# Kernel tuning notes

Hardware: AMD Instinct MI355X
Metric: run time of the kernel (lower is better)

Reference implementation:

```python
import jax, jax.numpy as jnp
import numpy as np

NC = 80            # num_classes
REG_MAX = 16
STRIDES = (8, 16, 32)
IMG = 640.0
TOPK = 10
TAL_ALPHA = 0.5
TAL_BETA = 6.0
L_BOX, L_CLS, L_DFL = 7.5, 0.5, 1.5
EPS = 1e-9
NEG = -1e8


def bbox_iou(b1, b2, ciou=False, eps=1e-7):
    # b1, b2: (..., 4) xyxy, broadcastable
    inter_wh = jnp.clip(jnp.minimum(b1[..., 2:], b2[..., 2:]) - jnp.maximum(b1[..., :2], b2[..., :2]), 0.0)
    inter = inter_wh[..., 0] * inter_wh[..., 1]
    w1 = jnp.clip(b1[..., 2] - b1[..., 0], 0.0); h1 = jnp.clip(b1[..., 3] - b1[..., 1], 0.0)
    w2 = jnp.clip(b2[..., 2] - b2[..., 0], 0.0); h2 = jnp.clip(b2[..., 3] - b2[..., 1], 0.0)
    union = w1 * h1 + w2 * h2 - inter + eps
    iou = inter / union
    if not ciou:
        return iou
    cx1 = (b1[..., 0] + b1[..., 2]) * 0.5; cy1 = (b1[..., 1] + b1[..., 3]) * 0.5
    cx2 = (b2[..., 0] + b2[..., 2]) * 0.5; cy2 = (b2[..., 1] + b2[..., 3]) * 0.5
    rho2 = (cx2 - cx1) ** 2 + (cy2 - cy1) ** 2
    cw = jnp.maximum(b1[..., 2], b2[..., 2]) - jnp.minimum(b1[..., 0], b2[..., 0])
    ch = jnp.maximum(b1[..., 3], b2[..., 3]) - jnp.minimum(b1[..., 1], b2[..., 1])
    c2 = cw ** 2 + ch ** 2 + eps
    v = (4.0 / np.pi ** 2) * (jnp.arctan(w2 / (h2 + eps)) - jnp.arctan(w1 / (h1 + eps))) ** 2
    alpha = jax.lax.stop_gradient(v / (1.0 - iou + v + eps))  # torch computes alpha under no_grad
    return iou - (rho2 / c2 + alpha * v)


def _assign_one(pred_scores, pred_bboxes, anchor_points, gt_labels, gt_bboxes):
    """TaskAlignedAssigner for one image.
    pred_scores (N,nc), pred_bboxes (N,4), anchor_points (N,2), gt_labels (M,), gt_bboxes (M,4).
    Returns target_bboxes (N,4), target_scores (N,nc), fg_mask (N,)."""
    N = pred_bboxes.shape[0]; M = gt_bboxes.shape[0]
    gl = jnp.clip(gt_labels.astype(jnp.int32), 0, NC - 1)
    x = anchor_points[:, 0]; y = anchor_points[:, 1]
    l = x[:, None] - gt_bboxes[None, :, 0]
    t = y[:, None] - gt_bboxes[None, :, 1]
    r = gt_bboxes[None, :, 2] - x[:, None]
    b = gt_bboxes[None, :, 3] - y[:, None]
    in_gts = (l > 0) & (t > 0) & (r > 0) & (b > 0)                     # (N,M)
    ious = bbox_iou(pred_bboxes[:, None, :], gt_bboxes[None, :, :])    # (N,M)
    cls_score = pred_scores[:, gl]                                     # (N,M)
    align = jnp.clip(cls_score, 0.0) ** TAL_ALPHA * jnp.clip(ious, 0.0) ** TAL_BETA
    align = jnp.where(in_gts, align, NEG)
    k = min(TOPK, N)
    _, topk_idx = jax.lax.top_k(align.T, k)                            # (M,k) indices into N
    mask_topk = jnp.zeros((M, N), dtype=bool).at[jnp.arange(M)[:, None], topk_idx].set(True).T
    mask_pos = mask_topk & in_gts                                      # (N,M)
    ious_pos = jnp.where(mask_pos, ious, -1.0)
    max_iou = ious_pos.max(axis=1)
    gt_idx = ious_pos.argmax(axis=1)                                   # (N,)
    fg_mask = max_iou > -0.5
    metric_pos = jnp.where(mask_pos, align, NEG)
    metric_max = jnp.clip(metric_pos.max(axis=0), EPS)                 # (M,)
    rows = jnp.arange(N)
    score = align[rows, gt_idx] / metric_max[gt_idx] * ious[rows, gt_idx]
    score = jnp.clip(score, 0.0, 1.0) * fg_mask.astype(pred_scores.dtype)
    tcls = gl[gt_idx]
    target_scores = jnp.zeros((N, NC), dtype=pred_scores.dtype).at[rows, tcls].set(score)
    target_bboxes = jnp.where(fg_mask[:, None], gt_bboxes[gt_idx], 0.0)
    return target_bboxes, target_scores, fg_mask


def _df_loss(reg_logits, target):
    # reg_logits (B,N,4,R) logits, target (B,N,4) float in [0,R-1] -> (B,N)
    t = jnp.clip(target, 0.0, float(REG_MAX - 1))
    left = jnp.floor(t).astype(jnp.int32)
    right = jnp.minimum(left + 1, REG_MAX - 1)
    wl = right.astype(t.dtype) - t
    wr = t - left.astype(t.dtype)
    same = right == left
    wl = jnp.where(same, 1.0, wl)
    wr = jnp.where(same, 0.0, wr)
    logp = jax.nn.log_softmax(reg_logits, axis=-1)
    ll = -jnp.take_along_axis(logp, left[..., None], axis=-1)[..., 0]
    lr = -jnp.take_along_axis(logp, right[..., None], axis=-1)[..., 0]
    return (ll * wl + lr * wr).sum(axis=-1)


def _forward(p0, p1, p2, gt_bboxes, gt_labels):
    preds = [p0, p1, p2]
    B = p0.shape[0]
    reg_ch = 4 * REG_MAX
    cls_list, reg_list, ap_list, st_list = [], [], [], []
    for p, s in zip(preds, STRIDES):
        _, _, h, w = p.shape
        reg = p[:, :reg_ch]
        cls = p[:, reg_ch:]
        cls_list.append(cls.transpose(0, 2, 3, 1).reshape(B, -1, NC))
        reg_list.append(reg.transpose(0, 2, 3, 1).reshape(B, -1, 4, REG_MAX))
        gy, gx = jnp.meshgrid(jnp.arange(h), jnp.arange(w), indexing='ij')
        pts = jnp.stack([(gx + 0.5) * s, (gy + 0.5) * s], axis=-1).reshape(-1, 2).astype(p.dtype)
        ap_list.append(pts)
        st_list.append(jnp.full((h * w,), float(s), dtype=p.dtype))
    cls_logits = jnp.concatenate(cls_list, axis=1)      # (B,N,nc)
    reg_logits = jnp.concatenate(reg_list, axis=1)      # (B,N,4,R)
    anchor_points = jnp.concatenate(ap_list, axis=0)    # (N,2)
    stride_t = jnp.concatenate(st_list, axis=0)         # (N,)
    pred_scores = jax.nn.sigmoid(cls_logits)
    proj = jnp.arange(REG_MAX, dtype=cls_logits.dtype)
    dist = (jax.nn.softmax(reg_logits, axis=-1) * proj).sum(-1) * stride_t[None, :, None]  # (B,N,4)
    ax = anchor_points[:, 0]; ay = anchor_points[:, 1]
    pred_bboxes = jnp.stack([ax - dist[..., 0], ay - dist[..., 1], ax + dist[..., 2], ay + dist[..., 3]], axis=-1)
    # --- TAL assignment (runs under no_grad in torch) ---
    tb, ts, fg = jax.vmap(lambda ps, pb, gl, gb: _assign_one(ps, pb, anchor_points, gl, gb))(
        jax.lax.stop_gradient(pred_scores), jax.lax.stop_gradient(pred_bboxes), gt_labels, gt_bboxes)
    tb = jax.lax.stop_gradient(tb)
    ts = jax.lax.stop_gradient(ts)
    ts_sum = jnp.maximum(ts.sum(), 1.0)
    # --- cls: BCE with logits over all anchors/classes ---
    z = cls_logits
    bce = jnp.clip(z, 0.0) - z * ts + jnp.log1p(jnp.exp(-jnp.abs(z)))
    loss_cls = bce.sum() / ts_sum
    # --- box: CIoU weighted by target score, fg only ---
    weight = ts.sum(-1) * fg.astype(ts.dtype)           # (B,N)
    ciou = bbox_iou(pred_bboxes, tb, ciou=True)         # (B,N)
    loss_box = ((1.0 - ciou) * weight).sum() / ts_sum
    # --- dfl ---
    inv_s = 1.0 / stride_t
    tl = (ax - tb[..., 0]) * inv_s
    tt = (ay - tb[..., 1]) * inv_s
    tr = (tb[..., 2] - ax) * inv_s
    tbm = (tb[..., 3] - ay) * inv_s
    target_ltrb = jnp.clip(jnp.stack([tl, tt, tr, tbm], axis=-1), 0.0, float(REG_MAX - 1))
    dfl = _df_loss(reg_logits, target_ltrb)             # (B,N)
    loss_dfl = (dfl * weight).sum() / ts_sum
    return L_BOX * loss_box + L_CLS * loss_cls + L_DFL * loss_dfl


def setup_inputs() -> dict:
    key = jax.random.key(0)
    k0, k1, k2, kc, kw, kl = jax.random.split(key, 6)
    B, C = 16, 4 * REG_MAX + NC
    p0 = jax.random.normal(k0, (B, C, 80, 80), dtype=jnp.float32)
    p1 = jax.random.normal(k1, (B, C, 40, 40), dtype=jnp.float32)
    p2 = jax.random.normal(k2, (B, C, 20, 20), dtype=jnp.float32)
    M = 32
    cxy = jax.random.uniform(kc, (B, M, 2), minval=64.0, maxval=IMG - 64.0)
    wh = jax.random.uniform(kw, (B, M, 2), minval=16.0, maxval=128.0)
    gt_bboxes = jnp.concatenate([cxy - wh * 0.5, cxy + wh * 0.5], axis=-1).astype(jnp.float32)
    gt_labels = jax.random.randint(kl, (B, M), 0, NC, dtype=jnp.int32).astype(jnp.int64)
    return {"p0": p0, "p1": p1, "p2": p2, "gt_bboxes": gt_bboxes, "gt_labels": gt_labels}


def reference(p0, p1, p2, gt_bboxes, gt_labels):
    return _forward(p0, p1, p2, gt_bboxes, gt_labels)
```

## Files before the change

### kernel.cpp

```cpp
#include <hip/hip_runtime.h>

#define BATCH 16
#define NANCH 8400
#define MGT 32
#define NCLS 80
#define RCH 64
#define NCH 144
#define TOPKK 10
#define MAXC 576
#define PBLK 2100
#define BCEB 2625
#define TOTB (PBLK + BCEB)

struct AInfo { int lvl, pos, W, HW; float s, ax, ay; };

__device__ __forceinline__ AInfo anchor_of(int n) {
  AInfo a;
  if (n < 6400)      { a.lvl = 0; a.pos = n;        a.W = 80; a.HW = 6400; a.s = 8.f;  }
  else if (n < 8000) { a.lvl = 1; a.pos = n - 6400; a.W = 40; a.HW = 1600; a.s = 16.f; }
  else               { a.lvl = 2; a.pos = n - 8000; a.W = 20; a.HW = 400;  a.s = 32.f; }
  int px = a.pos % a.W, py = a.pos / a.W;
  a.ax = (px + 0.5f) * a.s;
  a.ay = (py + 0.5f) * a.s;
  return a;
}

__device__ __forceinline__ const float* lvl_ptr(const float* p0, const float* p1,
                                                const float* p2, int lvl) {
  return lvl == 0 ? p0 : (lvl == 1 ? p1 : p2);
}

__device__ __forceinline__ float iou_xyxy(float4 a, float4 b) {
  float ix = fmaxf(fminf(a.z, b.z) - fmaxf(a.x, b.x), 0.f);
  float iy = fmaxf(fminf(a.w, b.w) - fmaxf(a.y, b.y), 0.f);
  float inter = ix * iy;
  float w1 = fmaxf(a.z - a.x, 0.f), h1 = fmaxf(a.w - a.y, 0.f);
  float w2 = fmaxf(b.z - b.x, 0.f), h2 = fmaxf(b.w - b.y, 0.f);
  float uni = w1 * h1 + w2 * h2 - inter + 1e-7f;
  return inter / uni;
}

__device__ __forceinline__ float ciou_xyxy(float4 a, float4 b) {
  const float eps = 1e-7f;
  float ix = fmaxf(fminf(a.z, b.z) - fmaxf(a.x, b.x), 0.f);
  float iy = fmaxf(fminf(a.w, b.w) - fmaxf(a.y, b.y), 0.f);
  float inter = ix * iy;
  float w1 = fmaxf(a.z - a.x, 0.f), h1 = fmaxf(a.w - a.y, 0.f);
  float w2 = fmaxf(b.z - b.x, 0.f), h2 = fmaxf(b.w - b.y, 0.f);
  float uni = w1 * h1 + w2 * h2 - inter + eps;
  float iou = inter / uni;
  float cx1 = (a.x + a.z) * 0.5f, cy1 = (a.y + a.w) * 0.5f;
  float cx2 = (b.x + b.z) * 0.5f, cy2 = (b.y + b.w) * 0.5f;
  float rho2 = (cx2 - cx1) * (cx2 - cx1) + (cy2 - cy1) * (cy2 - cy1);
  float cw = fmaxf(a.z, b.z) - fminf(a.x, b.x);
  float ch = fmaxf(a.w, b.w) - fminf(a.y, b.y);
  float c2 = cw * cw + ch * ch + eps;
  const float kpi = 4.f / (float)(M_PI * M_PI);
  float dat = atanf(w2 / (h2 + eps)) - atanf(w1 / (h1 + eps));
  float v = kpi * dat * dat;
  float alpha = v / (1.f - iou + v + eps);
  return iou - (rho2 / c2 + alpha * v);
}

__device__ __forceinline__ float block_sum256(float v) {
  __shared__ float sm[4];
  #pragma unroll
  for (int off = 32; off; off >>= 1) v += __shfl_xor(v, off);
  __syncthreads();
  if ((threadIdx.x & 63) == 0) sm[threadIdx.x >> 6] = v;
  __syncthreads();
  return (threadIdx.x == 0) ? (sm[0] + sm[1] + sm[2] + sm[3]) : 0.f;
}

__global__ __launch_bounds__(256) void k_fused(
    const float* __restrict__ p0, const float* __restrict__ p1, const float* __restrict__ p2,
    float* __restrict__ pboxf, float* __restrict__ logz,
    unsigned long long* __restrict__ slots, float* __restrict__ bce_part,
    double* __restrict__ accum) {
  int blk = blockIdx.x, tid = threadIdx.x;
  if (blk == 0 && tid < 8) accum[tid] = 0.0;

  if (blk < PBLK) {
    int q = blk & 3;
    int i = (blk >> 2) * 256 + tid;
    int b = i / NANCH, n = i % NANCH;
    AInfo A = anchor_of(n);
    const float* p = lvl_ptr(p0, p1, p2, A.lvl);
    size_t base = (size_t)b * NCH * A.HW + A.pos;

    float z[16]; float zm = -1e30f;
    #pragma unroll
    for (int j = 0; j < 16; ++j) {
      z[j] = p[base + (size_t)(q * 16 + j) * A.HW];
      zm = fmaxf(zm, z[j]);
    }
    float se = 0.f, ae = 0.f;
    #pragma unroll
    for (int j = 0; j < 16; ++j) {
      float e = __expf(z[j] - zm);
      se += e; ae += e * (float)j;
    }
    float d = ae / se * A.s;
    float val = (q == 0) ? A.ax - d : (q == 1) ? A.ay - d : (q == 2) ? A.ax + d : A.ay + d;
    pboxf[(size_t)i * 4 + q] = val;
    logz[(size_t)i * 4 + q] = zm + __logf(se);
    if (q == 0) slots[i] = 0ULL;
  } else {
    int r = blk - PBLK;
    int i = r * 256 + tid;
    float lb = 0.f;
    #pragma unroll
    for (int j = 0; j < 4; ++j) {
      int u = i + j * 672000;
      int b = u / 168000;
      int rr = u % 168000;
      const float4* src;
      if (rr < 128000)      src = (const float4*)p0 + ((size_t)(b * NCH + RCH) * 1600 + rr);
      else if (rr < 160000) src = (const float4*)p1 + ((size_t)(b * NCH + RCH) * 400 + (rr - 128000));
      else                  src = (const float4*)p2 + ((size_t)(b * NCH + RCH) * 100 + (rr - 160000));
      float4 z4 = *src;
      lb += fmaxf(z4.x, 0.f) + __logf(1.f + __expf(-fabsf(z4.x)));
      lb += fmaxf(z4.y, 0.f) + __logf(1.f + __expf(-fabsf(z4.y)));
      lb += fmaxf(z4.z, 0.f) + __logf(1.f + __expf(-fabsf(z4.z)));
      lb += fmaxf(z4.w, 0.f) + __logf(1.f + __expf(-fabsf(z4.w)));
    }
    float tot = block_sum256(lb);
    if (tid == 0) bce_part[r] = tot;
  }
}

__global__ __launch_bounds__(256) void k_topk(
    const float* __restrict__ p0, const float* __restrict__ p1, const float* __restrict__ p2,
    const float4* __restrict__ pbox, const float* __restrict__ gtb, const int* __restrict__ gtl,
    float* __restrict__ metric_max, unsigned long long* __restrict__ slots) {
  __shared__ float val[MAXC];
  __shared__ int   idx[MAXC];
  __shared__ float cio[MAXC];
  __shared__ float rv[4];
  __shared__ int   ri[4], rs[4], sdone[1];
  int b = blockIdx.x >> 5, m = blockIdx.x & 31;
  int tid = threadIdx.x;
  float4 g = ((const float4*)gtb)[b * MGT + m];
  int gl = min(max(gtl[b * MGT + m], 0), NCLS - 1);

  const int   Ws[3] = {80, 40, 20};
  const float ss[3] = {8.f, 16.f, 32.f};
  const int   nb[3] = {0, 6400, 8000};
  int x0[3], y0[3], nxl[3], cb[3];
  int cnt = 0;
  #pragma unroll
  for (int L = 0; L < 3; ++L) {
    float s = ss[L]; int W = Ws[L];
    int ax0 = max((int)floorf(g.x / s - 0.5f), 0);
    int ax1 = min((int)ceilf (g.z / s - 0.5f), W - 1);
    int ay0 = max((int)floorf(g.y / s - 0.5f), 0);
    int ay1 = min((int)ceilf (g.w / s - 0.5f), W - 1);
    int nx = max(ax1 - ax0 + 1, 0);
    int ny = max(ay1 - ay0 + 1, 0);
    x0[L] = ax0; y0[L] = ay0; nxl[L] = nx;
    cb[L] = cnt; cnt += nx * ny;
  }
  int C = min(cnt, MAXC);

  for (int t = tid; t < C; t += 256) {
    int L = (t >= cb[2]) ? 2 : (t >= cb[1]) ? 1 : 0;
    int r = t - cb[L];
    int ix = r % nxl[L], iy = r / nxl[L];
    int px = x0[L] + ix, py = y0[L] + iy;
    float ax = (px + 0.5f) * ss[L], ay = (py + 0.5f) * ss[L];
    float al = -3e38f, iou = 0.f; int n = 0x7fffffff;
    if (ax > g.x && ay > g.y && ax < g.z && ay < g.w) {
      n = nb[L] + py * Ws[L] + px;
      iou = iou_xyxy(pbox[(size_t)b * NANCH + n], g);
      int HW = (L == 0) ? 6400 : (L == 1) ? 1600 : 400;
      const float* p = lvl_ptr(p0, p1, p2, L);
      float z = p[(size_t)b * NCH * HW + (size_t)(RCH + gl) * HW + (py * Ws[L] + px)];
      float sg = 1.f / (1.f + __expf(-z));
      float i3 = iou * iou * iou;
      al = sqrtf(sg) * i3 * i3;
    }
    val[t] = al; idx[t] = n; cio[t] = iou;
  }
  __syncthreads();

  float mmax = -1.f;
  for (int k = 0; k < TOPKK; ++k) {
    float bv = -3e38f; int bn = 0x7fffffff, bs = 0;
    for (int t = tid; t < C; t += 256) {
      float v = val[t]; int n2 = idx[t];
      if (v > bv || (v == bv && n2 < bn)) { bv = v; bn = n2; bs = t; }
    }
    #pragma unroll
    for (int off = 32; off; off >>= 1) {
      float ov = __shfl_xor(bv, off);
      int   on = __shfl_xor(bn, off);
      int   os = __shfl_xor(bs, off);
      if (ov > bv || (ov == bv && on < bn)) { bv = ov; bn = on; bs = os; }
    }
    if ((tid & 63) == 0) { rv[tid >> 6] = bv; ri[tid >> 6] = bn; rs[tid >> 6] = bs; }
    __syncthreads();
    if (tid == 0) {
      #pragma unroll
      for (int w = 1; w < 4; ++w)
        if (rv[w] > bv || (rv[w] == bv && ri[w] < bn)) { bv = rv[w]; bn = ri[w]; bs = rs[w]; }
      if (bv >= 0.f) {
        mmax = fmaxf(mmax, bv);
        unsigned long long key = (1ULL << 62) |
                                 ((unsigned long long)__float_as_uint(cio[bs]) << 6) |
                                 (unsigned long long)(31 - m);
        atomicMax(&slots[(size_t)b * NANCH + bn], key);
        val[bs] = -3e38f;
        sdone[0] = 0;
      } else sdone[0] = 1;
    }
    __syncthreads();
    if (sdone[0]) break;
  }
  if (tid == 0) metric_max[b * MGT + m] = fmaxf(mmax, 1e-9f);
}

__global__ __launch_bounds__(256) void k_final(
    const float* __restrict__ p0, const float* __restrict__ p1, const float* __restrict__ p2,
    const float4* __restrict__ pbox, const float* __restrict__ logz,
    const float* __restrict__ gtb, const int* __restrict__ gtl,
    const float* __restrict__ metric_max, const unsigned long long* __restrict__ slots,
    double* __restrict__ accum) {
  int i = blockIdx.x * 256 + threadIdx.x;
  unsigned long long key = slots[i];
  float ts_p = 0.f, zc_p = 0.f, box_p = 0.f, dfl_p = 0.f;
  if (key) {
    int b = i / NANCH, n = i % NANCH;
    int m = 31 - (int)(key & 63ULL);
    float iou = __uint_as_float((unsigned int)((key >> 6) & 0xFFFFFFFFULL));
    AInfo A = anchor_of(n);
    float4 g = ((const float4*)gtb)[b * MGT + m];
    int gl = min(max(gtl[b * MGT + m], 0), NCLS - 1);
    const float* p = lvl_ptr(p0, p1, p2, A.lvl);
    size_t base = (size_t)b * NCH * A.HW + A.pos;

    float z = p[base + (size_t)(RCH + gl) * A.HW];
    float sg = 1.f / (1.f + __expf(-z));
    float i3 = iou * iou * iou;
    float align = sqrtf(sg) * i3 * i3;
    float mm = metric_max[b * MGT + m];
    float score = fminf(fmaxf(align / mm * iou, 0.f), 1.f);

    ts_p = score;
    zc_p = z * score;

    float4 pb = pbox[i];
    float ciou = ciou_xyxy(pb, g);
    box_p = (1.f - ciou) * score;

    float4 lz4 = ((const float4*)logz)[i];
    float inv_s = 1.f / A.s;
    float targ0 = (A.ax - g.x) * inv_s;
    float targ1 = (A.ay - g.y) * inv_s;
    float targ2 = (g.z - A.ax) * inv_s;
    float targ3 = (g.w - A.ay) * inv_s;
    float dfl = 0.f;
    #pragma unroll
    for (int sd = 0; sd < 4; ++sd) {
      float tg = sd == 0 ? targ0 : sd == 1 ? targ1 : sd == 2 ? targ2 : targ3;
      float lZ = sd == 0 ? lz4.x : sd == 1 ? lz4.y : sd == 2 ? lz4.z : lz4.w;
      float t = fminf(fmaxf(tg, 0.f), 15.f);
      int left = (int)floorf(t);
      int right = min(left + 1, 15);
      float wl, wr;
      if (right == left) { wl = 1.f; wr = 0.f; }
      else               { wl = (float)right - t; wr = t - (float)left; }
      float zl = p[base + (size_t)(sd * 16 + left)  * A.HW];
      float zr = p[base + (size_t)(sd * 16 + right) * A.HW];
      dfl += wl * (lZ - zl) + wr * (lZ - zr);
    }
    dfl_p = dfl * score;
  }
  float s;
  s = block_sum256(ts_p);  if (threadIdx.x == 0 && s != 0.f) atomicAdd(&accum[4], (double)s);
  s = block_sum256(zc_p);  if (threadIdx.x == 0 && s != 0.f) atomicAdd(&accum[1], (double)s);
  s = block_sum256(box_p); if (threadIdx.x == 0 && s != 0.f) atomicAdd(&accum[2], (double)s);
  s = block_sum256(dfl_p); if (threadIdx.x == 0 && s != 0.f) atomicAdd(&accum[3], (double)s);
}

__global__ void k_out(const double* __restrict__ accum, const float* __restrict__ bce_part,
                      float* __restrict__ out) {
  int tid = threadIdx.x;
  float s = 0.f;
  for (int t = tid; t < BCEB; t += 256) s += bce_part[t];
  s = block_sum256(s);
  if (tid == 0) {
    double ts = fmax(accum[4], 1.0);
    double loss = 7.5 * accum[2] / ts +
                  0.5 * ((double)s - accum[1]) / ts +
                  1.5 * accum[3] / ts;
    out[0] = (float)loss;
  }
}

extern "C" void kernel_launch(void* const* d_in, const int* in_sizes, int n_in,
                              void* d_out, int out_size, void* d_ws, size_t ws_size,
                              hipStream_t stream) {
  const float* p0  = (const float*)d_in[0];
  const float* p1  = (const float*)d_in[1];
  const float* p2  = (const float*)d_in[2];
  const float* gtb = (const float*)d_in[3];
  const int*   gtl = (const int*)d_in[4];
  float* out = (float*)d_out;

  char* ws = (char*)d_ws;
  double* accum      = (double*)ws;
  float*  metric_max = (float*)(ws + 64);
  float*  bce_part   = (float*)(ws + 2112);
  float*  pboxf      = (float*)(ws + 12624);
  float4* pbox       = (float4*)(ws + 12624);
  float*  logz       = (float*)(ws + 2163024);
  unsigned long long* slots = (unsigned long long*)(ws + 4313424);

  k_fused<<<TOTB, 256, 0, stream>>>(p0, p1, p2, pboxf, logz, slots, bce_part, accum);
  k_topk<<<BATCH * MGT, 256, 0, stream>>>(p0, p1, p2, pbox, gtb, gtl, metric_max, slots);
  k_final<<<(BATCH * NANCH) / 256, 256, 0, stream>>>(p0, p1, p2, pbox, logz, gtb, gtl,
                                                     metric_max, slots, accum);
  k_out<<<1, 256, 0, stream>>>(accum, bce_part, out);
}
```

Before: 149.3 us.

## Overlap BCE reduction with top-k assignment and fold final reduction into last block

Moves the class-logit BCE sum out of the first kernel and into the same launch as the per-GT top-k assignment, so the bandwidth-heavy BCE blocks run alongside the latency-bound 512 top-k blocks. BCE partials are now added with a double atomic instead of going to a partial buffer. The separate single-block output kernel is dropped: the last block of the final kernel, found through an atomic counter and a threadfence, computes the loss. This saves one launch and balances work across stages, at the cost of many double atomics on one address and a last-block-done pattern.

```diff
diff --git a/kernel.cpp b/kernel.cpp
--- a/kernel.cpp
+++ b/kernel.cpp
@@ -9,8 +9,9 @@
 #define TOPKK 10
 #define MAXC 576
 #define PBLK 2100
+#define TKB 512
 #define BCEB 2625
-#define TOTB (PBLK + BCEB)
+#define FINB 525
 
 struct AInfo { int lvl, pos, W, HW; float s, ax, ay; };
 
@@ -72,41 +73,56 @@
   return (threadIdx.x == 0) ? (sm[0] + sm[1] + sm[2] + sm[3]) : 0.f;
 }
 
-__global__ __launch_bounds__(256) void k_fused(
+__global__ __launch_bounds__(256) void k_pre(
     const float* __restrict__ p0, const float* __restrict__ p1, const float* __restrict__ p2,
     float* __restrict__ pboxf, float* __restrict__ logz,
-    unsigned long long* __restrict__ slots, float* __restrict__ bce_part,
+    unsigned long long* __restrict__ slots, double* __restrict__ accum,
+    int* __restrict__ counter) {
+  int blk = blockIdx.x, tid = threadIdx.x;
+  if (blk == 0) {
+    if (tid < 8) accum[tid] = 0.0;
+    if (tid == 8) *counter = 0;
+  }
+  int q = blk & 3;
+  int i = (blk >> 2) * 256 + tid;
+  int b = i / NANCH, n = i % NANCH;
+  AInfo A = anchor_of(n);
+  const float* p = lvl_ptr(p0, p1, p2, A.lvl);
+  size_t base = (size_t)b * NCH * A.HW + A.pos;
+
+  float z[16]; float zm = -1e30f;
+  #pragma unroll
+  for (int j = 0; j < 16; ++j) {
+    z[j] = p[base + (size_t)(q * 16 + j) * A.HW];
+    zm = fmaxf(zm, z[j]);
+  }
+  float se = 0.f, ae = 0.f;
+  #pragma unroll
+  for (int j = 0; j < 16; ++j) {
+    float e = __expf(z[j] - zm);
+    se += e; ae += e * (float)j;
+  }
+  float d = ae / se * A.s;
+  float val = (q == 0) ? A.ax - d : (q == 1) ? A.ay - d : (q == 2) ? A.ax + d : A.ay + d;
+  pboxf[(size_t)i * 4 + q] = val;
+  logz[(size_t)i * 4 + q] = zm + __logf(se);
+  if (q == 0) slots[i] = 0ULL;
+}
+
+__global__ __launch_bounds__(256) void k_mid(
+    const float* __restrict__ p0, const float* __restrict__ p1, const float* __restrict__ p2,
+    const float4* __restrict__ pbox, const float* __restrict__ gtb, const int* __restrict__ gtl,
+    float* __restrict__ metric_max, unsigned long long* __restrict__ slots,
     double* __restrict__ accum) {
+  __shared__ float val[MAXC];
+  __shared__ int   idx[MAXC];
+  __shared__ float cio[MAXC];
+  __shared__ float rv[4];
+  __shared__ int   ri[4], rs[4], sdone[1];
   int blk = blockIdx.x, tid = threadIdx.x;
-  if (blk == 0 && tid < 8) accum[tid] = 0.0;
-
-  if (blk < PBLK) {
-    int q = blk & 3;
-    int i = (blk >> 2) * 256 + tid;
-    int b = i / NANCH, n = i % NANCH;
-    AInfo A = anchor_of(n);
-    const float* p = lvl_ptr(p0, p1, p2, A.lvl);
-    size_t base = (size_t)b * NCH * A.HW + A.pos;
-
-    float z[16]; float zm = -1e30f;
-    #pragma unroll
-    for (int j = 0; j < 16; ++j) {
-      z[j] = p[base + (size_t)(q * 16 + j) * A.HW];
-      zm = fmaxf(zm, z[j]);
-    }
-    float se = 0.f, ae = 0.f;
-    #pragma unroll
-    for (int j = 0; j < 16; ++j) {
-      float e = __expf(z[j] - zm);
-      se += e; ae += e * (float)j;
-    }
-    float d = ae / se * A.s;
-    float val = (q == 0) ? A.ax - d : (q == 1) ? A.ay - d : (q == 2) ? A.ax + d : A.ay + d;
-    pboxf[(size_t)i * 4 + q] = val;
-    logz[(size_t)i * 4 + q] = zm + __logf(se);
-    if (q == 0) slots[i] = 0ULL;
-  } else {
-    int r = blk - PBLK;
+
+  if (blk >= TKB) {
+    int r = blk - TKB;
     int i = r * 256 + tid;
     float lb = 0.f;
     #pragma unroll
@@ -125,21 +141,11 @@
       lb += fmaxf(z4.w, 0.f) + __logf(1.f + __expf(-fabsf(z4.w)));
     }
     float tot = block_sum256(lb);
-    if (tid == 0) bce_part[r] = tot;
-  }
-}
-
-__global__ __launch_bounds__(256) void k_topk(
-    const float* __restrict__ p0, const float* __restrict__ p1, const float* __restrict__ p2,
-    const float4* __restrict__ pbox, const float* __restrict__ gtb, const int* __restrict__ gtl,
-    float* __restrict__ metric_max, unsigned long long* __restrict__ slots) {
-  __shared__ float val[MAXC];
-  __shared__ int   idx[MAXC];
-  __shared__ float cio[MAXC];
-  __shared__ float rv[4];
-  __shared__ int   ri[4], rs[4], sdone[1];
-  int b = blockIdx.x >> 5, m = blockIdx.x & 31;
-  int tid = threadIdx.x;
+    if (tid == 0) atomicAdd(&accum[0], (double)tot);
+    return;
+  }
+
+  int b = blk >> 5, m = blk & 31;
   float4 g = ((const float4*)gtb)[b * MGT + m];
   int gl = min(max(gtl[b * MGT + m], 0), NCLS - 1);
 
@@ -224,7 +230,7 @@
     const float4* __restrict__ pbox, const float* __restrict__ logz,
     const float* __restrict__ gtb, const int* __restrict__ gtl,
     const float* __restrict__ metric_max, const unsigned long long* __restrict__ slots,
-    double* __restrict__ accum) {
+    double* __restrict__ accum, int* __restrict__ counter, float* __restrict__ out) {
   int i = blockIdx.x * 256 + threadIdx.x;
   unsigned long long key = slots[i];
   float ts_p = 0.f, zc_p = 0.f, box_p = 0.f, dfl_p = 0.f;
@@ -280,20 +286,19 @@
   s = block_sum256(zc_p);  if (threadIdx.x == 0 && s != 0.f) atomicAdd(&accum[1], (double)s);
   s = block_sum256(box_p); if (threadIdx.x == 0 && s != 0.f) atomicAdd(&accum[2], (double)s);
   s = block_sum256(dfl_p); if (threadIdx.x == 0 && s != 0.f) atomicAdd(&accum[3], (double)s);
-}
-
-__global__ void k_out(const double* __restrict__ accum, const float* __restrict__ bce_part,
-                      float* __restrict__ out) {
-  int tid = threadIdx.x;
-  float s = 0.f;
-  for (int t = tid; t < BCEB; t += 256) s += bce_part[t];
-  s = block_sum256(s);
-  if (tid == 0) {
-    double ts = fmax(accum[4], 1.0);
-    double loss = 7.5 * accum[2] / ts +
-                  0.5 * ((double)s - accum[1]) / ts +
-                  1.5 * accum[3] / ts;
-    out[0] = (float)loss;
+
+  __threadfence();
+  __shared__ int last;
+  if (threadIdx.x == 0) last = (atomicAdd(counter, 1) == FINB - 1);
+  __syncthreads();
+  if (last && threadIdx.x == 0) {
+    double a0 = atomicAdd(&accum[0], 0.0);
+    double a1 = atomicAdd(&accum[1], 0.0);
+    double a2 = atomicAdd(&accum[2], 0.0);
+    double a3 = atomicAdd(&accum[3], 0.0);
+    double a4 = atomicAdd(&accum[4], 0.0);
+    double ts = fmax(a4, 1.0);
+    out[0] = (float)(7.5 * a2 / ts + 0.5 * (a0 - a1) / ts + 1.5 * a3 / ts);
   }
 }
 
@@ -309,16 +314,15 @@
 
   char* ws = (char*)d_ws;
   double* accum      = (double*)ws;
-  float*  metric_max = (float*)(ws + 64);
-  float*  bce_part   = (float*)(ws + 2112);
-  float*  pboxf      = (float*)(ws + 12624);
-  float4* pbox       = (float4*)(ws + 12624);
-  float*  logz       = (float*)(ws + 2163024);
-  unsigned long long* slots = (unsigned long long*)(ws + 4313424);
-
-  k_fused<<<TOTB, 256, 0, stream>>>(p0, p1, p2, pboxf, logz, slots, bce_part, accum);
-  k_topk<<<BATCH * MGT, 256, 0, stream>>>(p0, p1, p2, pbox, gtb, gtl, metric_max, slots);
-  k_final<<<(BATCH * NANCH) / 256, 256, 0, stream>>>(p0, p1, p2, pbox, logz, gtb, gtl,
-                                                     metric_max, slots, accum);
-  k_out<<<1, 256, 0, stream>>>(accum, bce_part, out);
-}
+  int*    counter    = (int*)(ws + 64);
+  float*  metric_max = (float*)(ws + 80);
+  float*  pboxf      = (float*)(ws + 2128);
+  float4* pbox       = (float4*)(ws + 2128);
+  float*  logz       = (float*)(ws + 2152528);
+  unsigned long long* slots = (unsigned long long*)(ws + 4302928);
+
+  k_pre<<<PBLK, 256, 0, stream>>>(p0, p1, p2, pboxf, logz, slots, accum, counter);
+  k_mid<<<TKB + BCEB, 256, 0, stream>>>(p0, p1, p2, pbox, gtb, gtl, metric_max, slots, accum);
+  k_final<<<FINB, 256, 0, stream>>>(p0, p1, p2, pbox, logz, gtb, gtl,
+                                    metric_max, slots, accum, counter, out);
+}
```

Result: slower. 193.5 us (+29.6%).
